# Kernel tuning notes

Measured on AMD Instinct MI355X. Metric: run time of the kernel, lower is better.

Reference implementation:

```python
import jax, jax.numpy as jnp
import numpy as np

OMEGA_0 = 30.0  # SIREN frequency from init_kwargs


def setup_inputs() -> dict:
    key = jax.random.key(0)
    ks = jax.random.split(key, 8)
    B, Cin, Cout, H, L = 64, 64, 64, 128, 8192
    return {
        "x": jax.random.normal(ks[0], (B, Cin, L), dtype=jnp.float32),
        "w1": jax.random.normal(ks[1], (H, 1), dtype=jnp.float32) * (1.0 / 1.0),
        "b1": jax.random.normal(ks[2], (H,), dtype=jnp.float32) * 0.1,
        "w2": jax.random.normal(ks[3], (H, H), dtype=jnp.float32) * (1.0 / np.sqrt(H)),
        "b2": jax.random.normal(ks[4], (H,), dtype=jnp.float32) * 0.1,
        "w3": jax.random.normal(ks[5], (Cout * Cin, H), dtype=jnp.float32) * (1.0 / np.sqrt(H)),
        "b3": jax.random.normal(ks[6], (Cout * Cin,), dtype=jnp.float32) * 0.1,
        "bias": jnp.zeros((Cout,), dtype=jnp.float32),
    }


def reference(x, w1, b1, w2, b2, w3, b3, bias):
    B, Cin, L = x.shape
    Cout = bias.shape[0]
    # 1. relative positions in [-1, 1], one per input timestep
    rel = jnp.linspace(-1.0, 1.0, L)  # [L]
    # 2. SIREN kernel-generating MLP (1x1 convs over positions == per-position MLP)
    h = jnp.sin(OMEGA_0 * (rel[:, None] * w1[:, 0][None, :] + b1))       # [L, H]
    h = jnp.sin(OMEGA_0 * (h @ w2.T + b2))                               # [L, H]
    k = h @ w3.T + b3                                                    # [L, Cout*Cin]
    # torch: Kernel output [1, Cout*Cin, L].view(Cout, Cin, L)
    kernel = k.T.reshape(Cout, Cin, L)                                   # [Cout, Cin, L]
    # 3. conv1d with padding=0 and kernel length == L -> single output position
    #    (cross-correlation, exactly torch.nn.functional.conv1d)
    out = jnp.einsum("bil,oil->bo", x, kernel) + bias                    # [B, Cout]
    return out[:, :, None]                                               # [B, Cout, 1]
```

## Files before the change

kernel.cpp:

```cpp
#include <hip/hip_runtime.h>
#include <hip/hip_bf16.h>

#define LPOS 8192
#define HDIM 128
#define M_TOT 4096
#define GROW  136
#define GELEMS (M_TOT * GROW)
#define KSPLIT 16
#define CUNITS 1024
#define BUNITS (4 * CUNITS)
#define NPART 256

typedef float  f32x4 __attribute__((ext_vector_type(4)));
typedef short  s16x8 __attribute__((ext_vector_type(8)));
typedef unsigned int u32x4 __attribute__((ext_vector_type(4)));

__device__ __forceinline__ unsigned short bf16_rne(float f) {
    unsigned u = __builtin_bit_cast(unsigned, f);
    u += 0x7fffu + ((u >> 16) & 1u);
    return (unsigned short)(u >> 16);
}
__device__ __forceinline__ float bf16f(unsigned short v) {
    return __builtin_bit_cast(float, (unsigned)v << 16);
}

__device__ __forceinline__ s16x8 cvt8(f32x4 a, f32x4 b) {
    s16x8 r;
    r[0] = (short)bf16_rne(a[0]); r[1] = (short)bf16_rne(a[1]);
    r[2] = (short)bf16_rne(a[2]); r[3] = (short)bf16_rne(a[3]);
    r[4] = (short)bf16_rne(b[0]); r[5] = (short)bf16_rne(b[1]);
    r[6] = (short)bf16_rne(b[2]); r[7] = (short)bf16_rne(b[3]);
    return r;
}

__device__ __forceinline__ float sum8(f32x4 a, f32x4 b) {
    return ((a[0] + a[1]) + (a[2] + a[3])) + ((b[0] + b[1]) + (b[2] + b[3]));
}

__global__ __launch_bounds__(256) void k1_siren(
        const float* __restrict__ w1, const float* __restrict__ b1,
        const float* __restrict__ w2, const float* __restrict__ b2,
        unsigned short* __restrict__ h2T) {
    __shared__ float w2sT[HDIM * 129];
    __shared__ __align__(16) float h1s[2][HDIM * 8];
    const int tid = threadIdx.x;
    const int s = tid >> 7;
    const int h = tid & 127;

    for (int idx = tid; idx < HDIM * HDIM; idx += 256)
        w2sT[(idx & 127) * 129 + (idx >> 7)] = w2[idx];

    const int l0 = blockIdx.x * 16 + s * 8;
    const float myw1 = w1[h], myb1 = b1[h];
    #pragma unroll
    for (int ls = 0; ls < 8; ++ls) {
        float rel = -1.0f + (2.0f / 8191.0f) * (float)(l0 + ls);
        h1s[s][h * 8 + ls] = __sinf(30.0f * (rel * myw1 + myb1));
    }
    __syncthreads();

    const float bb = b2[h];
    float acc[8];
    #pragma unroll
    for (int ls = 0; ls < 8; ++ls) acc[ls] = bb;

    for (int j = 0; j < HDIM; ++j) {
        float wv = w2sT[j * 129 + h];
        const f32x4* hp = (const f32x4*)&h1s[s][j * 8];
        f32x4 p0 = hp[0], p1 = hp[1];
        acc[0] += wv * p0[0]; acc[1] += wv * p0[1];
        acc[2] += wv * p0[2]; acc[3] += wv * p0[3];
        acc[4] += wv * p1[0]; acc[5] += wv * p1[1];
        acc[6] += wv * p1[2]; acc[7] += wv * p1[3];
    }

    u32x4 ov;
    #pragma unroll
    for (int q = 0; q < 4; ++q) {
        unsigned lo = bf16_rne(__sinf(30.0f * acc[2 * q]));
        unsigned hi = bf16_rne(__sinf(30.0f * acc[2 * q + 1]));
        ov[q] = lo | (hi << 16);
    }
    const size_t c = (size_t)(l0 >> 6);
    const int k8 = (l0 >> 3) & 7;
    *(u32x4*)(h2T + (c * CUNITS + (size_t)k8 * 128 + h) * 8) = ov;
}

__global__ __launch_bounds__(256, 2) void k2_gemm(
        const float* __restrict__ x, const unsigned short* __restrict__ h2T,
        unsigned short* __restrict__ gp) {
    __shared__ unsigned short lds[BUNITS * 8];

    const int lane = threadIdx.x & 63;
    const int wv   = threadIdx.x >> 6;
    const int r    = lane & 15;
    const int kg   = lane >> 4;
    const int m0   = blockIdx.x * 128;
    const int y8   = blockIdx.y;
    const int kc   = y8 * 512;

    const float* xpa = x + (size_t)(m0 + wv * 32 + r) * LPOS + kc + kg * 8;
    const float* xpb = xpa + 16 * LPOS;

    f32x4 xr[2][2][4];

#define LOADX(SL, IT) do { \
        xr[SL][0][0] = *(const f32x4*)(xpa + (IT) * 64);      \
        xr[SL][0][1] = *(const f32x4*)(xpa + (IT) * 64 + 4);  \
        xr[SL][0][2] = *(const f32x4*)(xpa + (IT) * 64 + 32); \
        xr[SL][0][3] = *(const f32x4*)(xpa + (IT) * 64 + 36); \
        xr[SL][1][0] = *(const f32x4*)(xpb + (IT) * 64);      \
        xr[SL][1][1] = *(const f32x4*)(xpb + (IT) * 64 + 4);  \
        xr[SL][1][2] = *(const f32x4*)(xpb + (IT) * 64 + 32); \
        xr[SL][1][3] = *(const f32x4*)(xpb + (IT) * 64 + 36); \
    } while (0)

    f32x4 acc[2][8];
    #pragma unroll
    for (int s = 0; s < 2; ++s)
        #pragma unroll
        for (int t = 0; t < 8; ++t) { f32x4 z = {0.f,0.f,0.f,0.f}; acc[s][t] = z; }
    float sacc0 = 0.f, sacc1 = 0.f;

    #pragma unroll 1
    for (int g = 0; g < 2; ++g) {
        const int base = g * 4;
        {
            const unsigned short* src = h2T + (size_t)(y8 * 2 + g) * (BUNITS * 8);
            #pragma unroll
            for (int j = 0; j < 16; ++j) {
                const int U = j * 256 + threadIdx.x;
                __builtin_amdgcn_global_load_lds(
                    (const unsigned int*)(src + (size_t)U * 8),
                    (unsigned int*)&lds[U * 8], 16, 0, 0);
            }
        }
        LOADX(0, base); LOADX(1, base + 1);
        __syncthreads();

        #pragma unroll
        for (int it = 0; it < 4; ++it) {
            const int sl = it & 1;
            s16x8 a0lo = cvt8(xr[sl][0][0], xr[sl][0][1]);
            s16x8 a0hi = cvt8(xr[sl][0][2], xr[sl][0][3]);
            s16x8 a1lo = cvt8(xr[sl][1][0], xr[sl][1][1]);
            s16x8 a1hi = cvt8(xr[sl][1][2], xr[sl][1][3]);
            sacc0 += sum8(xr[sl][0][0], xr[sl][0][1]) + sum8(xr[sl][0][2], xr[sl][0][3]);
            sacc1 += sum8(xr[sl][1][0], xr[sl][1][1]) + sum8(xr[sl][1][2], xr[sl][1][3]);
            if (it + 2 < 4) LOADX(sl, base + it + 2);

            #pragma unroll
            for (int t = 0; t < 8; ++t) {
                s16x8 blo = *(const s16x8*)&lds[((size_t)it * CUNITS + kg * 128 + t * 16 + r) * 8];
                s16x8 bhi = *(const s16x8*)&lds[((size_t)it * CUNITS + (kg + 4) * 128 + t * 16 + r) * 8];
                acc[0][t] = __builtin_amdgcn_mfma_f32_16x16x32_bf16(a0lo, blo, acc[0][t], 0, 0, 0);
                acc[0][t] = __builtin_amdgcn_mfma_f32_16x16x32_bf16(a0hi, bhi, acc[0][t], 0, 0, 0);
                acc[1][t] = __builtin_amdgcn_mfma_f32_16x16x32_bf16(a1lo, blo, acc[1][t], 0, 0, 0);
                acc[1][t] = __builtin_amdgcn_mfma_f32_16x16x32_bf16(a1hi, bhi, acc[1][t], 0, 0, 0);
            }
        }
        __syncthreads();
    }
#undef LOADX

    unsigned short* gpy = gp + (size_t)y8 * GELEMS;
    #pragma unroll
    for (int s = 0; s < 2; ++s) {
        #pragma unroll
        for (int t = 0; t < 8; ++t) {
            const int col = t * 16 + r;
            #pragma unroll
            for (int q = 0; q < 4; ++q) {
                const int row = m0 + wv * 32 + s * 16 + kg * 4 + q;
                gpy[(size_t)row * GROW + col] = bf16_rne(acc[s][t][q]);
            }
        }
    }
    sacc0 += __shfl_xor(sacc0, 16); sacc0 += __shfl_xor(sacc0, 32);
    sacc1 += __shfl_xor(sacc1, 16); sacc1 += __shfl_xor(sacc1, 32);
    if (kg == 0) {
        gpy[(size_t)(m0 + wv * 32 + r) * GROW + 128]      = bf16_rne(sacc0);
        gpy[(size_t)(m0 + wv * 32 + 16 + r) * GROW + 128] = bf16_rne(sacc1);
    }
}

__global__ __launch_bounds__(256, 3) void k3_mm(
        const unsigned short* __restrict__ gp, const float* __restrict__ w3,
        const float* __restrict__ b3, float* __restrict__ part) {
    __shared__ unsigned short As[2][64 * 128];
    __shared__ unsigned short Bs[64 * 128];
    __shared__ float b3s[64];
    __shared__ float sls[64];

    const int bid = blockIdx.x;
    const int i   = bid >> 2;
    const int y0  = (bid & 3) * 4;
    const int t    = threadIdx.x;
    const int lane = t & 63;
    const int w    = t >> 6;
    const int r    = lane & 15;
    const int kg   = lane >> 4;

    #pragma unroll
    for (int p = 0; p < 4; ++p) {
        const int row  = p * 16 + (t >> 4);
        const int gran = t & 15;
        const float* src = w3 + (size_t)(row * 64 + i) * HDIM + gran * 8;
        f32x4 v0 = *(const f32x4*)src;
        f32x4 v1 = *(const f32x4*)(src + 4);
        *(s16x8*)&Bs[row * 128 + ((gran ^ (row & 7)) * 8)] = cvt8(v0, v1);
    }
    if (t < 64) b3s[t] = b3[t * 64 + i];

    float sreg = 0.f;
    auto stageA = [&](int y, int d) {
        const unsigned short* src = gp + (size_t)y * GELEMS + (size_t)i * GROW;
        #pragma unroll
        for (int p = 0; p < 4; ++p) {
            const int b    = p * 16 + (t >> 4);
            const int gran = t & 15;
            s16x8 v = *(const s16x8*)(src + (size_t)b * (64 * GROW) + gran * 8);
            *(s16x8*)&As[d][b * 128 + ((gran ^ (b & 7)) * 8)] = v;
        }
        if (t < 64) sreg += bf16f(src[(size_t)t * (64 * GROW) + 128]);
    };

    stageA(y0, 0);
    __syncthreads();

    s16x8 bfr[4][4];
    #pragma unroll
    for (int ct = 0; ct < 4; ++ct) {
        const int o = ct * 16 + r;
        #pragma unroll
        for (int ks = 0; ks < 4; ++ks)
            bfr[ct][ks] = *(const s16x8*)&Bs[o * 128 + (((ks * 4 + kg) ^ (o & 7)) * 8)];
    }

    f32x4 acc[4];
    #pragma unroll
    for (int ct = 0; ct < 4; ++ct) { f32x4 z = {0.f,0.f,0.f,0.f}; acc[ct] = z; }

    const int bA = w * 16 + r;
    #pragma unroll
    for (int yy = 0; yy < 4; ++yy) {
        if (yy + 1 < 4) stageA(y0 + yy + 1, (yy + 1) & 1);
        const unsigned short* buf = &As[yy & 1][0];
        s16x8 af[4];
        #pragma unroll
        for (int ks = 0; ks < 4; ++ks)
            af[ks] = *(const s16x8*)&buf[bA * 128 + (((ks * 4 + kg) ^ (bA & 7)) * 8)];
        #pragma unroll
        for (int ct = 0; ct < 4; ++ct)
            #pragma unroll
            for (int ks = 0; ks < 4; ++ks)
                acc[ct] = __builtin_amdgcn_mfma_f32_16x16x32_bf16(af[ks], bfr[ct][ks], acc[ct], 0, 0, 0);
        __syncthreads();
    }

    if (t < 64) sls[t] = sreg;
    __syncthreads();

    float* po = part + (size_t)bid * 4096;
    #pragma unroll
    for (int ct = 0; ct < 4; ++ct) {
        const int o = ct * 16 + r;
        #pragma unroll
        for (int q = 0; q < 4; ++q) {
            const int b = w * 16 + kg * 4 + q;
            po[b * 64 + o] = acc[ct][q] + sls[b] * b3s[o];
        }
    }
}

__global__ __launch_bounds__(256) void k4_final(
        const float* __restrict__ part, const float* __restrict__ bias,
        float* __restrict__ out) {
    const int idx = blockIdx.x * 256 + threadIdx.x;
    float s = bias[idx & 63];
    #pragma unroll 8
    for (int p = 0; p < NPART; ++p)
        s += part[(size_t)p * 4096 + idx];
    out[idx] = s;
}

extern "C" void kernel_launch(void* const* d_in, const int* in_sizes, int n_in,
                              void* d_out, int out_size, void* d_ws, size_t ws_size,
                              hipStream_t stream) {
    (void)in_sizes; (void)n_in; (void)out_size; (void)ws_size;
    const float* x    = (const float*)d_in[0];
    const float* w1   = (const float*)d_in[1];
    const float* b1   = (const float*)d_in[2];
    const float* w2   = (const float*)d_in[3];
    const float* b2   = (const float*)d_in[4];
    const float* w3   = (const float*)d_in[5];
    const float* b3   = (const float*)d_in[6];
    const float* bias = (const float*)d_in[7];
    float* out = (float*)d_out;

    char* ws = (char*)d_ws;
    unsigned short* h2T = (unsigned short*)ws;
    const size_t H2T_BYTES = (size_t)(LPOS / 64) * CUNITS * 16;
    unsigned short* gp = (unsigned short*)(ws + H2T_BYTES);
    const size_t GP_BYTES = (size_t)KSPLIT * GELEMS * 2;
    float* part = (float*)(ws + H2T_BYTES + GP_BYTES);

    k1_siren<<<LPOS / 16, 256, 0, stream>>>(w1, b1, w2, b2, h2T);
    k2_gemm<<<dim3(M_TOT / 128, KSPLIT), 256, 0, stream>>>(x, h2T, gp);
    k3_mm<<<NPART, 256, 0, stream>>>(gp, w3, b3, part);
    k4_final<<<16, 256, 0, stream>>>(part, bias, out);
}
```

Before: 66.13 us.

## Fuse final partial reduction into k3 via last-block atomic counter

Removes the separate k4_final launch. The output is now initialised to bias inside k1, and each group of four k3 blocks uses an atomic counter so the last block to finish sums the group's four partials and atomically adds them into the output. This saves one kernel launch and the serial 256-partial read loop that ran on only 16 blocks. In exchange it adds fences, float atomics with a non-deterministic summation order, and depends on k1 resetting the counters on every call.

```diff
diff --git a/kernel.cpp b/kernel.cpp
--- a/kernel.cpp
+++ b/kernel.cpp
@@ -40,12 +40,19 @@
 __global__ __launch_bounds__(256) void k1_siren(
         const float* __restrict__ w1, const float* __restrict__ b1,
         const float* __restrict__ w2, const float* __restrict__ b2,
-        unsigned short* __restrict__ h2T) {
+        const float* __restrict__ bias,
+        unsigned short* __restrict__ h2T, float* __restrict__ out,
+        unsigned* __restrict__ cnt) {
     __shared__ float w2sT[HDIM * 129];
     __shared__ __align__(16) float h1s[2][HDIM * 8];
     const int tid = threadIdx.x;
     const int s = tid >> 7;
     const int h = tid & 127;
+
+    if (blockIdx.x == 0) {
+        for (int idx = tid; idx < 4096; idx += 256) out[idx] = bias[idx & 63];
+        if (tid < 64) cnt[tid] = 0;
+    }
 
     for (int idx = tid; idx < HDIM * HDIM; idx += 256)
         w2sT[(idx & 127) * 129 + (idx >> 7)] = w2[idx];
@@ -186,11 +193,13 @@
 
 __global__ __launch_bounds__(256, 3) void k3_mm(
         const unsigned short* __restrict__ gp, const float* __restrict__ w3,
-        const float* __restrict__ b3, float* __restrict__ part) {
+        const float* __restrict__ b3, float* __restrict__ part,
+        float* __restrict__ out, unsigned* __restrict__ cnt) {
     __shared__ unsigned short As[2][64 * 128];
     __shared__ unsigned short Bs[64 * 128];
     __shared__ float b3s[64];
     __shared__ float sls[64];
+    __shared__ int is_last;
 
     const int bid = blockIdx.x;
     const int i   = bid >> 2;
@@ -271,17 +280,27 @@
             po[b * 64 + o] = acc[ct][q] + sls[b] * b3s[o];
         }
     }
-}
-
-__global__ __launch_bounds__(256) void k4_final(
-        const float* __restrict__ part, const float* __restrict__ bias,
-        float* __restrict__ out) {
-    const int idx = blockIdx.x * 256 + threadIdx.x;
-    float s = bias[idx & 63];
-    #pragma unroll 8
-    for (int p = 0; p < NPART; ++p)
-        s += part[(size_t)p * 4096 + idx];
-    out[idx] = s;
+
+    __syncthreads();
+    if (t == 0) {
+        __threadfence();
+        unsigned old = __hip_atomic_fetch_add(&cnt[i], 1u, __ATOMIC_ACQ_REL,
+                                              __HIP_MEMORY_SCOPE_AGENT);
+        is_last = (old == 3u);
+    }
+    __syncthreads();
+    if (is_last) {
+        const float* p0 = part + (size_t)(i * 4 + 0) * 4096;
+        const float* p1 = part + (size_t)(i * 4 + 1) * 4096;
+        const float* p2 = part + (size_t)(i * 4 + 2) * 4096;
+        const float* p3 = part + (size_t)(i * 4 + 3) * 4096;
+        #pragma unroll
+        for (int n = 0; n < 16; ++n) {
+            const int idx = n * 256 + t;
+            float s = (p0[idx] + p1[idx]) + (p2[idx] + p3[idx]);
+            unsafeAtomicAdd(&out[idx], s);
+        }
+    }
 }
 
 extern "C" void kernel_launch(void* const* d_in, const int* in_sizes, int n_in,
@@ -304,9 +323,10 @@
     unsigned short* gp = (unsigned short*)(ws + H2T_BYTES);
     const size_t GP_BYTES = (size_t)KSPLIT * GELEMS * 2;
     float* part = (float*)(ws + H2T_BYTES + GP_BYTES);
-
-    k1_siren<<<LPOS / 16, 256, 0, stream>>>(w1, b1, w2, b2, h2T);
+    const size_t PART_BYTES = (size_t)NPART * 4096 * 4;
+    unsigned* cnt = (unsigned*)(ws + H2T_BYTES + GP_BYTES + PART_BYTES);
+
+    k1_siren<<<LPOS / 16, 256, 0, stream>>>(w1, b1, w2, b2, bias, h2T, out, cnt);
     k2_gemm<<<dim3(M_TOT / 128, KSPLIT), 256, 0, stream>>>(x, h2T, gp);
-    k3_mm<<<NPART, 256, 0, stream>>>(gp, w3, b3, part);
-    k4_final<<<16, 256, 0, stream>>>(part, bias, out);
-}
+    k3_mm<<<NPART, 256, 0, stream>>>(gp, w3, b3, part, out, cnt);
+}
```

Result: slower. 74.58 us (+12.8%).

## Fuse x·h2 GEMM with w3 contraction per input channel, drop intermediate buffer

Applied to the files above, without the earlier changes.

The k2 GEMM and k3 w3-contraction are merged into one kernel. Each block handles one input channel i and one K-split chunk, so the bf16 G intermediate stays in LDS instead of going through global memory. The partial-sum count grows from 256 to 1024, and k4 is reworked to split the reduction across four wave groups. In exchange, each block now reloads and converts a w3 slice, and the final reduction reads four times more partials.

```diff
diff --git a/kernel.cpp b/kernel.cpp
--- a/kernel.cpp
+++ b/kernel.cpp
@@ -4,12 +4,10 @@
 #define LPOS 8192
 #define HDIM 128
 #define M_TOT 4096
-#define GROW  136
-#define GELEMS (M_TOT * GROW)
 #define KSPLIT 16
 #define CUNITS 1024
 #define BUNITS (4 * CUNITS)
-#define NPART 256
+#define NPART 1024
 
 typedef float  f32x4 __attribute__((ext_vector_type(4)));
 typedef short  s16x8 __attribute__((ext_vector_type(8)));
@@ -19,9 +17,6 @@
     unsigned u = __builtin_bit_cast(unsigned, f);
     u += 0x7fffu + ((u >> 16) & 1u);
     return (unsigned short)(u >> 16);
-}
-__device__ __forceinline__ float bf16f(unsigned short v) {
-    return __builtin_bit_cast(float, (unsigned)v << 16);
 }
 
 __device__ __forceinline__ s16x8 cvt8(f32x4 a, f32x4 b) {
@@ -86,41 +81,36 @@
     *(u32x4*)(h2T + (c * CUNITS + (size_t)k8 * 128 + h) * 8) = ov;
 }
 
-__global__ __launch_bounds__(256, 2) void k2_gemm(
+__global__ __launch_bounds__(256, 2) void k2_fused(
         const float* __restrict__ x, const unsigned short* __restrict__ h2T,
-        unsigned short* __restrict__ gp) {
-    __shared__ unsigned short lds[BUNITS * 8];
-
-    const int lane = threadIdx.x & 63;
-    const int wv   = threadIdx.x >> 6;
+        const float* __restrict__ w3, const float* __restrict__ b3,
+        float* __restrict__ part) {
+    __shared__ __align__(16) char smem[65536];
+    unsigned short* lds = (unsigned short*)smem;
+
+    const int t    = threadIdx.x;
+    const int lane = t & 63;
+    const int wv   = t >> 6;
     const int r    = lane & 15;
     const int kg   = lane >> 4;
-    const int m0   = blockIdx.x * 128;
+    const int i    = blockIdx.x;
     const int y8   = blockIdx.y;
     const int kc   = y8 * 512;
 
-    const float* xpa = x + (size_t)(m0 + wv * 32 + r) * LPOS + kc + kg * 8;
-    const float* xpb = xpa + 16 * LPOS;
-
-    f32x4 xr[2][2][4];
-
+    const float* xp = x + (size_t)((wv * 16 + r) * 64 + i) * LPOS + kc + kg * 8;
+
+    f32x4 xr[2][4];
 #define LOADX(SL, IT) do { \
-        xr[SL][0][0] = *(const f32x4*)(xpa + (IT) * 64);      \
-        xr[SL][0][1] = *(const f32x4*)(xpa + (IT) * 64 + 4);  \
-        xr[SL][0][2] = *(const f32x4*)(xpa + (IT) * 64 + 32); \
-        xr[SL][0][3] = *(const f32x4*)(xpa + (IT) * 64 + 36); \
-        xr[SL][1][0] = *(const f32x4*)(xpb + (IT) * 64);      \
-        xr[SL][1][1] = *(const f32x4*)(xpb + (IT) * 64 + 4);  \
-        xr[SL][1][2] = *(const f32x4*)(xpb + (IT) * 64 + 32); \
-        xr[SL][1][3] = *(const f32x4*)(xpb + (IT) * 64 + 36); \
+        xr[SL][0] = *(const f32x4*)(xp + (IT) * 64);      \
+        xr[SL][1] = *(const f32x4*)(xp + (IT) * 64 + 4);  \
+        xr[SL][2] = *(const f32x4*)(xp + (IT) * 64 + 32); \
+        xr[SL][3] = *(const f32x4*)(xp + (IT) * 64 + 36); \
     } while (0)
 
-    f32x4 acc[2][8];
-    #pragma unroll
-    for (int s = 0; s < 2; ++s)
-        #pragma unroll
-        for (int t = 0; t < 8; ++t) { f32x4 z = {0.f,0.f,0.f,0.f}; acc[s][t] = z; }
-    float sacc0 = 0.f, sacc1 = 0.f;
+    f32x4 acc[8];
+    #pragma unroll
+    for (int t8 = 0; t8 < 8; ++t8) { f32x4 z = {0.f,0.f,0.f,0.f}; acc[t8] = z; }
+    float sacc = 0.f;
 
     #pragma unroll 1
     for (int g = 0; g < 2; ++g) {
@@ -129,7 +119,7 @@
             const unsigned short* src = h2T + (size_t)(y8 * 2 + g) * (BUNITS * 8);
             #pragma unroll
             for (int j = 0; j < 16; ++j) {
-                const int U = j * 256 + threadIdx.x;
+                const int U = j * 256 + t;
                 __builtin_amdgcn_global_load_lds(
                     (const unsigned int*)(src + (size_t)U * 8),
                     (unsigned int*)&lds[U * 8], 16, 0, 0);
@@ -141,65 +131,40 @@
         #pragma unroll
         for (int it = 0; it < 4; ++it) {
             const int sl = it & 1;
-            s16x8 a0lo = cvt8(xr[sl][0][0], xr[sl][0][1]);
-            s16x8 a0hi = cvt8(xr[sl][0][2], xr[sl][0][3]);
-            s16x8 a1lo = cvt8(xr[sl][1][0], xr[sl][1][1]);
-            s16x8 a1hi = cvt8(xr[sl][1][2], xr[sl][1][3]);
-            sacc0 += sum8(xr[sl][0][0], xr[sl][0][1]) + sum8(xr[sl][0][2], xr[sl][0][3]);
-            sacc1 += sum8(xr[sl][1][0], xr[sl][1][1]) + sum8(xr[sl][1][2], xr[sl][1][3]);
+            s16x8 alo = cvt8(xr[sl][0], xr[sl][1]);
+            s16x8 ahi = cvt8(xr[sl][2], xr[sl][3]);
+            sacc += sum8(xr[sl][0], xr[sl][1]) + sum8(xr[sl][2], xr[sl][3]);
             if (it + 2 < 4) LOADX(sl, base + it + 2);
 
             #pragma unroll
-            for (int t = 0; t < 8; ++t) {
-                s16x8 blo = *(const s16x8*)&lds[((size_t)it * CUNITS + kg * 128 + t * 16 + r) * 8];
-                s16x8 bhi = *(const s16x8*)&lds[((size_t)it * CUNITS + (kg + 4) * 128 + t * 16 + r) * 8];
-                acc[0][t] = __builtin_amdgcn_mfma_f32_16x16x32_bf16(a0lo, blo, acc[0][t], 0, 0, 0);
-                acc[0][t] = __builtin_amdgcn_mfma_f32_16x16x32_bf16(a0hi, bhi, acc[0][t], 0, 0, 0);
-                acc[1][t] = __builtin_amdgcn_mfma_f32_16x16x32_bf16(a1lo, blo, acc[1][t], 0, 0, 0);
-                acc[1][t] = __builtin_amdgcn_mfma_f32_16x16x32_bf16(a1hi, bhi, acc[1][t], 0, 0, 0);
+            for (int t8 = 0; t8 < 8; ++t8) {
+                s16x8 blo = *(const s16x8*)&lds[((size_t)it * CUNITS + kg * 128 + t8 * 16 + r) * 8];
+                s16x8 bhi = *(const s16x8*)&lds[((size_t)it * CUNITS + (kg + 4) * 128 + t8 * 16 + r) * 8];
+                acc[t8] = __builtin_amdgcn_mfma_f32_16x16x32_bf16(alo, blo, acc[t8], 0, 0, 0);
+                acc[t8] = __builtin_amdgcn_mfma_f32_16x16x32_bf16(ahi, bhi, acc[t8], 0, 0, 0);
             }
         }
         __syncthreads();
     }
 #undef LOADX
 
-    unsigned short* gpy = gp + (size_t)y8 * GELEMS;
-    #pragma unroll
-    for (int s = 0; s < 2; ++s) {
-        #pragma unroll
-        for (int t = 0; t < 8; ++t) {
-            const int col = t * 16 + r;
-            #pragma unroll
-            for (int q = 0; q < 4; ++q) {
-                const int row = m0 + wv * 32 + s * 16 + kg * 4 + q;
-                gpy[(size_t)row * GROW + col] = bf16_rne(acc[s][t][q]);
-            }
-        }
-    }
-    sacc0 += __shfl_xor(sacc0, 16); sacc0 += __shfl_xor(sacc0, 32);
-    sacc1 += __shfl_xor(sacc1, 16); sacc1 += __shfl_xor(sacc1, 32);
-    if (kg == 0) {
-        gpy[(size_t)(m0 + wv * 32 + r) * GROW + 128]      = bf16_rne(sacc0);
-        gpy[(size_t)(m0 + wv * 32 + 16 + r) * GROW + 128] = bf16_rne(sacc1);
-    }
-}
-
-__global__ __launch_bounds__(256, 3) void k3_mm(
-        const unsigned short* __restrict__ gp, const float* __restrict__ w3,
-        const float* __restrict__ b3, float* __restrict__ part) {
-    __shared__ unsigned short As[2][64 * 128];
-    __shared__ unsigned short Bs[64 * 128];
-    __shared__ float b3s[64];
-    __shared__ float sls[64];
-
-    const int bid = blockIdx.x;
-    const int i   = bid >> 2;
-    const int y0  = (bid & 3) * 4;
-    const int t    = threadIdx.x;
-    const int lane = t & 63;
-    const int w    = t >> 6;
-    const int r    = lane & 15;
-    const int kg   = lane >> 4;
+    unsigned short* As = (unsigned short*)smem;
+    unsigned short* Bs = (unsigned short*)(smem + 16384);
+    float* b3s = (float*)(smem + 32768);
+    float* sls = (float*)(smem + 33024);
+
+    #pragma unroll
+    for (int t8 = 0; t8 < 8; ++t8) {
+        const int col = t8 * 16 + r;
+        const int cg = col >> 3, cw = col & 7;
+        #pragma unroll
+        for (int q = 0; q < 4; ++q) {
+            const int b = wv * 16 + kg * 4 + q;
+            As[b * 128 + ((cg ^ (b & 7)) * 8) + cw] = bf16_rne(acc[t8][q]);
+        }
+    }
+    sacc += __shfl_xor(sacc, 16); sacc += __shfl_xor(sacc, 32);
+    if (kg == 0) sls[wv * 16 + r] = sacc;
 
     #pragma unroll
     for (int p = 0; p < 4; ++p) {
@@ -211,21 +176,6 @@
         *(s16x8*)&Bs[row * 128 + ((gran ^ (row & 7)) * 8)] = cvt8(v0, v1);
     }
     if (t < 64) b3s[t] = b3[t * 64 + i];
-
-    float sreg = 0.f;
-    auto stageA = [&](int y, int d) {
-        const unsigned short* src = gp + (size_t)y * GELEMS + (size_t)i * GROW;
-        #pragma unroll
-        for (int p = 0; p < 4; ++p) {
-            const int b    = p * 16 + (t >> 4);
-            const int gran = t & 15;
-            s16x8 v = *(const s16x8*)(src + (size_t)b * (64 * GROW) + gran * 8);
-            *(s16x8*)&As[d][b * 128 + ((gran ^ (b & 7)) * 8)] = v;
-        }
-        if (t < 64) sreg += bf16f(src[(size_t)t * (64 * GROW) + 128]);
-    };
-
-    stageA(y0, 0);
     __syncthreads();
 
     s16x8 bfr[4][4];
@@ -236,39 +186,29 @@
         for (int ks = 0; ks < 4; ++ks)
             bfr[ct][ks] = *(const s16x8*)&Bs[o * 128 + (((ks * 4 + kg) ^ (o & 7)) * 8)];
     }
-
-    f32x4 acc[4];
-    #pragma unroll
-    for (int ct = 0; ct < 4; ++ct) { f32x4 z = {0.f,0.f,0.f,0.f}; acc[ct] = z; }
-
-    const int bA = w * 16 + r;
-    #pragma unroll
-    for (int yy = 0; yy < 4; ++yy) {
-        if (yy + 1 < 4) stageA(y0 + yy + 1, (yy + 1) & 1);
-        const unsigned short* buf = &As[yy & 1][0];
-        s16x8 af[4];
+    const int bA = wv * 16 + r;
+    s16x8 af[4];
+    #pragma unroll
+    for (int ks = 0; ks < 4; ++ks)
+        af[ks] = *(const s16x8*)&As[bA * 128 + (((ks * 4 + kg) ^ (bA & 7)) * 8)];
+
+    f32x4 acc2[4];
+    #pragma unroll
+    for (int ct = 0; ct < 4; ++ct) { f32x4 z = {0.f,0.f,0.f,0.f}; acc2[ct] = z; }
+    #pragma unroll
+    for (int ct = 0; ct < 4; ++ct)
         #pragma unroll
         for (int ks = 0; ks < 4; ++ks)
-            af[ks] = *(const s16x8*)&buf[bA * 128 + (((ks * 4 + kg) ^ (bA & 7)) * 8)];
-        #pragma unroll
-        for (int ct = 0; ct < 4; ++ct)
-            #pragma unroll
-            for (int ks = 0; ks < 4; ++ks)
-                acc[ct] = __builtin_amdgcn_mfma_f32_16x16x32_bf16(af[ks], bfr[ct][ks], acc[ct], 0, 0, 0);
-        __syncthreads();
-    }
-
-    if (t < 64) sls[t] = sreg;
-    __syncthreads();
-
-    float* po = part + (size_t)bid * 4096;
+            acc2[ct] = __builtin_amdgcn_mfma_f32_16x16x32_bf16(af[ks], bfr[ct][ks], acc2[ct], 0, 0, 0);
+
+    float* po = part + ((size_t)i * 16 + y8) * 4096;
     #pragma unroll
     for (int ct = 0; ct < 4; ++ct) {
         const int o = ct * 16 + r;
         #pragma unroll
         for (int q = 0; q < 4; ++q) {
-            const int b = w * 16 + kg * 4 + q;
-            po[b * 64 + o] = acc[ct][q] + sls[b] * b3s[o];
+            const int b = wv * 16 + kg * 4 + q;
+            po[b * 64 + o] = acc2[ct][q] + sls[b] * b3s[o];
         }
     }
 }
@@ -276,12 +216,20 @@
 __global__ __launch_bounds__(256) void k4_final(
         const float* __restrict__ part, const float* __restrict__ bias,
         float* __restrict__ out) {
-    const int idx = blockIdx.x * 256 + threadIdx.x;
-    float s = bias[idx & 63];
+    __shared__ float red[4][64];
+    const int t  = threadIdx.x;
+    const int il = t & 63;
+    const int pg = t >> 6;
+    const int idx = blockIdx.x * 64 + il;
+
+    float s = 0.f;
     #pragma unroll 8
-    for (int p = 0; p < NPART; ++p)
+    for (int p = pg * 256; p < pg * 256 + 256; ++p)
         s += part[(size_t)p * 4096 + idx];
-    out[idx] = s;
+    red[pg][il] = s;
+    __syncthreads();
+    if (t < 64)
+        out[blockIdx.x * 64 + t] = bias[t] + ((red[0][t] + red[1][t]) + (red[2][t] + red[3][t]));
 }
 
 extern "C" void kernel_launch(void* const* d_in, const int* in_sizes, int n_in,
@@ -301,12 +249,9 @@
     char* ws = (char*)d_ws;
     unsigned short* h2T = (unsigned short*)ws;
     const size_t H2T_BYTES = (size_t)(LPOS / 64) * CUNITS * 16;
-    unsigned short* gp = (unsigned short*)(ws + H2T_BYTES);
-    const size_t GP_BYTES = (size_t)KSPLIT * GELEMS * 2;
-    float* part = (float*)(ws + H2T_BYTES + GP_BYTES);
+    float* part = (float*)(ws + H2T_BYTES);
 
     k1_siren<<<LPOS / 16, 256, 0, stream>>>(w1, b1, w2, b2, h2T);
-    k2_gemm<<<dim3(M_TOT / 128, KSPLIT), 256, 0, stream>>>(x, h2T, gp);
-    k3_mm<<<NPART, 256, 0, stream>>>(gp, w3, b3, part);
-    k4_final<<<16, 256, 0, stream>>>(part, bias, out);
-}
+    k2_fused<<<dim3(64, KSPLIT), 256, 0, stream>>>(x, h2T, w3, b3, part);
+    k4_final<<<64, 256, 0, stream>>>(part, bias, out);
+}
```

Result: faster. 59.89 us (-9.4%).
